# Performance work log

Measured on AMD Instinct MI355X. Metric: run time of the kernel, lower is better.

## Reference

```python
import jax, jax.numpy as jnp
import numpy as np

N_NODES = 1000000
N_EDGES = 2000000
N_FEAT = 11          # QM9 num_features
HIDDEN = 64
N_CLASSES = 19       # QM9 num_classes
BATCH = 128


def setup_inputs() -> dict:
    key = jax.random.key(0)
    k = jax.random.split(key, 8)
    x = jax.random.normal(k[0], (N_NODES, N_FEAT), dtype=jnp.float32)
    edge_index = jax.random.randint(k[1], (2, N_EDGES), 0, N_NODES, dtype=jnp.int64)
    y = jax.random.normal(k[2], (BATCH, N_CLASSES), dtype=jnp.float32)
    batch = jnp.sort(jax.random.randint(k[3], (N_NODES,), 0, BATCH, dtype=jnp.int64))
    # GCNConv params: weight [in, hidden], bias [hidden]
    W_conv = jax.random.normal(k[4], (N_FEAT, HIDDEN), dtype=jnp.float32) / np.sqrt(N_FEAT)
    b_conv = jnp.zeros((HIDDEN,), dtype=jnp.float32)
    # Final linear: [hidden, classes]
    W_lin = jax.random.normal(k[5], (HIDDEN, N_CLASSES), dtype=jnp.float32) / np.sqrt(HIDDEN)
    b_lin = jnp.zeros((N_CLASSES,), dtype=jnp.float32)
    return {"x": x, "edge_index": edge_index, "y": y, "batch": batch,
            "W_conv": W_conv, "b_conv": b_conv, "W_lin": W_lin, "b_lin": b_lin}


def reference(x, edge_index, y, batch, W_conv, b_conv, W_lin, b_lin):
    row, col = edge_index[0], edge_index[1]  # source -> target
    # GCN symmetric normalization (add_self_loops=False): deg over targets
    ones = jnp.ones((edge_index.shape[1],), dtype=x.dtype)
    deg = jax.ops.segment_sum(ones, col, num_segments=N_NODES)
    dinv = jnp.where(deg > 0, jax.lax.rsqrt(jnp.maximum(deg, 1.0)), 0.0)
    norm = dinv[row] * dinv[col]  # [E]
    # Transform then aggregate: gather at source, scatter-add at target
    xw = x @ W_conv                                    # [N, H]
    msgs = xw[row] * norm[:, None]                     # [E, H]
    agg = jax.ops.segment_sum(msgs, col, num_segments=N_NODES) + b_conv
    h = jax.nn.relu(agg)                               # [N, H]
    # global_mean_pool over batch ids (size=BATCH)
    summed = jax.ops.segment_sum(h, batch, num_segments=BATCH)   # [B, H]
    counts = jax.ops.segment_sum(jnp.ones((N_NODES,), dtype=x.dtype), batch, num_segments=BATCH)
    pooled = summed / jnp.maximum(counts, 1.0)[:, None]
    # dropout p=0.5 is identity in eval mode
    return pooled @ W_lin + b_lin                      # [B, classes]
```

## Files before the change

### kernel.cpp

```cpp
#include <hip/hip_runtime.h>

#define N_NODES   1000000
#define N_EDGES   2000000
#define N_FEAT    11
#define HIDDEN    64
#define BATCH     128
#define N_CLASSES 19

#define NPB     2048
#define NBUCK   489
#define BCAP    5120
#define EPB     8192
#define PBLK    245
#define NSLOT   8
#define NCHUNK  3907
#define FSTR    12

__device__ __forceinline__ unsigned f2b(float v) {
    unsigned u = __float_as_uint(v);
    return (u + 0x7FFFu + ((u >> 16) & 1u)) >> 16;
}

__global__ __launch_bounds__(1024) void part_kernel(const int* __restrict__ row,
                                                    const int* __restrict__ col,
                                                    int* __restrict__ bcnt,
                                                    int* __restrict__ part) {
    __shared__ int lh[512];
    const int t = threadIdx.x;
    if (t < 512) lh[t] = 0;
    __syncthreads();
    const int q0 = (blockIdx.x * EPB) >> 2;
    const int4* col4 = (const int4*)col;
    const int4* row4 = (const int4*)row;
    const int qa = q0 + t, qb = q0 + 1024 + t;
    const bool va = qa < N_EDGES / 4, vb = qb < N_EDGES / 4;
    int4 ca, ra, cb, rb;
    if (va) { ca = col4[qa]; ra = row4[qa]; }
    if (vb) { cb = col4[qb]; rb = row4[qb]; }
    if (va) {
        atomicAdd(&lh[ca.x >> 11], 1); atomicAdd(&lh[ca.y >> 11], 1);
        atomicAdd(&lh[ca.z >> 11], 1); atomicAdd(&lh[ca.w >> 11], 1);
    }
    if (vb) {
        atomicAdd(&lh[cb.x >> 11], 1); atomicAdd(&lh[cb.y >> 11], 1);
        atomicAdd(&lh[cb.z >> 11], 1); atomicAdd(&lh[cb.w >> 11], 1);
    }
    __syncthreads();
    if (t < NBUCK) {
        int v = lh[t];
        if (v) lh[t] = t * BCAP + atomicAdd(&bcnt[t], v);
    }
    __syncthreads();
    int p;
    if (va) {
        p = atomicAdd(&lh[ca.x >> 11], 1); part[p] = (ra.x << 11) | (ca.x & (NPB - 1));
        p = atomicAdd(&lh[ca.y >> 11], 1); part[p] = (ra.y << 11) | (ca.y & (NPB - 1));
        p = atomicAdd(&lh[ca.z >> 11], 1); part[p] = (ra.z << 11) | (ca.z & (NPB - 1));
        p = atomicAdd(&lh[ca.w >> 11], 1); part[p] = (ra.w << 11) | (ca.w & (NPB - 1));
    }
    if (vb) {
        p = atomicAdd(&lh[cb.x >> 11], 1); part[p] = (rb.x << 11) | (cb.x & (NPB - 1));
        p = atomicAdd(&lh[cb.y >> 11], 1); part[p] = (rb.y << 11) | (cb.y & (NPB - 1));
        p = atomicAdd(&lh[cb.z >> 11], 1); part[p] = (rb.z << 11) | (cb.z & (NPB - 1));
        p = atomicAdd(&lh[cb.w >> 11], 1); part[p] = (rb.w << 11) | (cb.w & (NPB - 1));
    }
}

__global__ __launch_bounds__(512) void sort2_kernel(const int* __restrict__ part,
                                                    const int* __restrict__ bcnt,
                                                    const float* __restrict__ x,
                                                    int* __restrict__ srcs,
                                                    int* __restrict__ nstart,
                                                    unsigned short* __restrict__ ndeg,
                                                    float* __restrict__ dinv,
                                                    unsigned short* __restrict__ xs) {
    __shared__ int cnt[NPB];
    __shared__ int off[NPB];
    __shared__ int tsum[512];
    __shared__ int stage[BCAP];
    const int t = threadIdx.x, b = blockIdx.x;
    for (int i = t; i < NPB; i += 512) cnt[i] = 0;
    __syncthreads();
    const int s0 = b * BCAP, e0 = s0 + bcnt[b];
    for (int j = s0 + t; j < e0; j += 512)
        atomicAdd(&cnt[part[j] & (NPB - 1)], 1);
    __syncthreads();
    const int i0 = t * 4;
    int c[4], s = 0;
#pragma unroll
    for (int q = 0; q < 4; ++q) { c[q] = cnt[i0 + q]; s += c[q]; }
    tsum[t] = s;
    __syncthreads();
    for (int o = 1; o < 512; o <<= 1) {
        int a = (t >= o) ? tsum[t - o] : 0;
        __syncthreads();
        tsum[t] += a;
        __syncthreads();
    }
    int run = tsum[t] - s;
#pragma unroll
    for (int q = 0; q < 4; ++q) { off[i0 + q] = run; run += c[q]; }
    __syncthreads();
    for (int i = t; i < NPB; i += 512) {
        int n = b * NPB + i;
        if (n < N_NODES) {
            int d = cnt[i];
            float dv = d ? rsqrtf((float)d) : 0.0f;
            dinv[n]   = dv;
            ndeg[n]   = (unsigned short)d;
            nstart[n] = s0 + off[i];
            const float* xr = x + (size_t)n * N_FEAT;
            unsigned h[11];
#pragma unroll
            for (int k = 0; k < 11; ++k) h[k] = f2b(dv * xr[k]);
            uint4 A, B;
            A.x = h[0] | (h[1] << 16); A.y = h[2] | (h[3] << 16);
            A.z = h[4] | (h[5] << 16); A.w = h[6] | (h[7] << 16);
            B.x = h[8] | (h[9] << 16); B.y = h[10]; B.z = 0u; B.w = 0u;
            uint4* o = (uint4*)(xs + (size_t)n * 16);
            o[0] = A; o[1] = B;
        }
    }
    __syncthreads();
    for (int j = s0 + t; j < e0; j += 512) {
        int p  = part[j];
        int cl = p & (NPB - 1);
        int pos = atomicAdd(&off[cl], 1);
        stage[pos] = p >> 11;
    }
    __syncthreads();
    const int m = e0 - s0;
    const int m4 = m >> 2;
    int4* d4 = (int4*)(srcs + s0);
    const int4* s4 = (const int4*)stage;
    for (int j = t; j < m4; j += 512) d4[j] = s4[j];
    for (int j = (m4 << 2) + t; j < m; j += 512) srcs[s0 + j] = stage[j];
}

__global__ __launch_bounds__(256) void gather_pool_kernel(
    const int* __restrict__ srcs, const unsigned short* __restrict__ xs,
    const int* __restrict__ nstart, const unsigned short* __restrict__ ndeg,
    const float* __restrict__ dinv, const int* __restrict__ batch,
    const float* __restrict__ Wc, const float* __restrict__ bc,
    float* __restrict__ pooled, float* __restrict__ countsf) {
    __shared__ float facc[256 * FSTR];
    __shared__ int   sj0[256];
    __shared__ int   sdeg[256];
    __shared__ float sdinv[256];
    __shared__ int   sbid[256];
    __shared__ int   sperm[256];
    __shared__ int   dcnt[32];
    __shared__ int   doff[32];
    __shared__ float pbuf[NSLOT * HIDDEN];
    __shared__ int   pcnt[NSLOT];
    const int t = threadIdx.x, lane = t & 63, w = t >> 6;
    const int base = blockIdx.x * 256;
    {
        int n = base + t;
        bool v = n < N_NODES;
        sj0[t]   = v ? nstart[n] : 0;
        sdeg[t]  = v ? (int)ndeg[n] : 0;
        sdinv[t] = v ? dinv[n] : 0.0f;
        sbid[t]  = v ? batch[n] : -1;
    }
    for (int i = t; i < NSLOT * HIDDEN; i += 256) pbuf[i] = 0.0f;
    if (t < NSLOT) pcnt[t] = 0;
    if (t < 32)    dcnt[t] = 0;
    __syncthreads();
    int mybin = sdeg[t] < 31 ? sdeg[t] : 31;
    atomicAdd(&dcnt[mybin], 1);
    __syncthreads();
    if (t < 32) {
        int r = 0;
        for (int i = 0; i < t; ++i) r += dcnt[i];
        doff[t] = r;
    }
    __syncthreads();
    int pos = atomicAdd(&doff[mybin], 1);
    sperm[pos] = t;
    __syncthreads();

    {
        int i  = sperm[t];
        int j0 = sj0[i], d = sdeg[i];
        float acc[11];
#pragma unroll
        for (int k = 0; k < 11; ++k) acc[k] = 0.0f;
        for (int j = j0; j < j0 + d; ++j) {
            int r = srcs[j];
            const uint4* xr = (const uint4*)(xs + (size_t)r * 16);
            uint4 A = xr[0];
            uint2 B = *(const uint2*)(xr + 1);
            acc[0]  += __uint_as_float(A.x << 16);
            acc[1]  += __uint_as_float(A.x & 0xFFFF0000u);
            acc[2]  += __uint_as_float(A.y << 16);
            acc[3]  += __uint_as_float(A.y & 0xFFFF0000u);
            acc[4]  += __uint_as_float(A.z << 16);
            acc[5]  += __uint_as_float(A.z & 0xFFFF0000u);
            acc[6]  += __uint_as_float(A.w << 16);
            acc[7]  += __uint_as_float(A.w & 0xFFFF0000u);
            acc[8]  += __uint_as_float(B.x << 16);
            acc[9]  += __uint_as_float(B.x & 0xFFFF0000u);
            acc[10] += __uint_as_float(B.y << 16);
        }
        float* f = &facc[i * FSTR];
#pragma unroll
        for (int k = 0; k < 11; ++k) f[k] = acc[k];
    }
    __syncthreads();

    float wk[N_FEAT];
#pragma unroll
    for (int k = 0; k < N_FEAT; ++k) wk[k] = Wc[k * HIDDEN + lane];
    const float bias = bc[lane];
    const int bid0 = sbid[0];
    int cur = -1; float accp = 0.0f; int cntp = 0;
    for (int i = w * 64; i < w * 64 + 64; ++i) {
        int bid = sbid[i];
        if (bid < 0) break;
        if (bid != cur) {
            if (cur >= 0) {
                int slot = cur - bid0;
                if (slot >= 0 && slot < NSLOT) {
                    atomicAdd(&pbuf[slot * HIDDEN + lane], accp);
                    if (lane == 0) atomicAdd(&pcnt[slot], cntp);
                } else {
                    atomicAdd(&pooled[(size_t)cur * HIDDEN + lane], accp);
                    if (lane == 0) atomicAdd(&countsf[cur], (float)cntp);
                }
            }
            cur = bid; accp = 0.0f; cntp = 0;
        }
        float s = 0.0f;
#pragma unroll
        for (int k = 0; k < N_FEAT; ++k)
            s = fmaf(wk[k], facc[i * FSTR + k], s);
        accp += fmaxf(fmaf(sdinv[i], s, bias), 0.0f);
        ++cntp;
    }
    if (cur >= 0) {
        int slot = cur - bid0;
        if (slot >= 0 && slot < NSLOT) {
            atomicAdd(&pbuf[slot * HIDDEN + lane], accp);
            if (lane == 0) atomicAdd(&pcnt[slot], cntp);
        } else {
            atomicAdd(&pooled[(size_t)cur * HIDDEN + lane], accp);
            if (lane == 0) atomicAdd(&countsf[cur], (float)cntp);
        }
    }
    __syncthreads();
    for (int s = w; s < NSLOT; s += 4) {
        int c = pcnt[s];
        if (c > 0) {
            atomicAdd(&pooled[(size_t)(bid0 + s) * HIDDEN + lane], pbuf[s * HIDDEN + lane]);
            if (lane == 0) atomicAdd(&countsf[bid0 + s], (float)c);
        }
    }
}

__global__ void final_kernel(const float* __restrict__ pooled, const float* __restrict__ counts,
                             const float* __restrict__ Wl, const float* __restrict__ bl,
                             float* __restrict__ out) {
    int i = blockIdx.x * blockDim.x + threadIdx.x;
    if (i >= BATCH * N_CLASSES) return;
    int b = i / N_CLASSES;
    int c = i - b * N_CLASSES;
    float inv = 1.0f / fmaxf(counts[b], 1.0f);
    float s = bl[c];
#pragma unroll 8
    for (int h = 0; h < HIDDEN; ++h)
        s = fmaf(pooled[b * HIDDEN + h] * inv, Wl[h * N_CLASSES + c], s);
    out[i] = s;
}

extern "C" void kernel_launch(void* const* d_in, const int* in_sizes, int n_in,
                              void* d_out, int out_size, void* d_ws, size_t ws_size,
                              hipStream_t stream) {
    const float* x     = (const float*)d_in[0];
    const int*   ei    = (const int*)d_in[1];
    const int*   batch = (const int*)d_in[3];
    const float* Wc    = (const float*)d_in[4];
    const float* bc    = (const float*)d_in[5];
    const float* Wl    = (const float*)d_in[6];
    const float* bl    = (const float*)d_in[7];
    float*       out   = (float*)d_out;

    int*            bcnt    = (int*)d_ws;
    float*          pooled  = (float*)(bcnt + 512);
    float*          countsf = pooled + BATCH * HIDDEN;
    unsigned short* xs      = (unsigned short*)(countsf + BATCH);
    int*            nstart  = (int*)(xs + (size_t)N_NODES * 16);
    unsigned short* ndeg    = (unsigned short*)(nstart + N_NODES);
    float*          dinv    = (float*)(ndeg + N_NODES);
    int*            part    = (int*)(dinv + N_NODES);
    int*            srcs    = part + (size_t)NBUCK * BCAP;

    size_t zero_bytes = (512 + BATCH * HIDDEN + BATCH) * 4;
    hipMemsetAsync(d_ws, 0, zero_bytes, stream);

    const int* row = ei;
    const int* col = ei + N_EDGES;

    part_kernel <<<PBLK, 1024, 0, stream>>>(row, col, bcnt, part);
    sort2_kernel<<<NBUCK, 512, 0, stream>>>(part, bcnt, x, srcs, nstart, ndeg, dinv, xs);
    gather_pool_kernel<<<NCHUNK, 256, 0, stream>>>(srcs, xs, nstart, ndeg, dinv,
                                                   batch, Wc, bc, pooled, countsf);
    final_kernel<<<(BATCH * N_CLASSES + 255) / 256, 256, 0, stream>>>(pooled, countsf, Wl, bl, out);
}
```

Before: 230.7 us.

## Compute per-node GCN transform with bf16 MFMA instead of scalar FMA loop

The per-block dense transform (aggregated 11 features times the 11x64 weight) now uses 16x16x32 bf16 MFMA tiles, with aggregated features packed to bf16 in shared memory and weights converted to bf16 per lane. Node counts are accumulated up front per node instead of per run. Pooling changes from per-wave run-length accumulation to per-element atomics into shared or global buffers, one atomic per node and channel. This adds bf16 rounding of the aggregates and weights, and many more atomics, in exchange for removing the scalar dot-product loop.

```diff
diff --git a/kernel.cpp b/kernel.cpp
--- a/kernel.cpp
+++ b/kernel.cpp
@@ -14,7 +14,11 @@
 #define PBLK    245
 #define NSLOT   8
 #define NCHUNK  3907
-#define FSTR    12
+#define FROW    24
+#define ZOFF    (256 * FROW)
+
+typedef __attribute__((ext_vector_type(8))) short v8s;
+typedef __attribute__((ext_vector_type(4))) float v4f;
 
 __device__ __forceinline__ unsigned f2b(float v) {
     unsigned u = __float_as_uint(v);
@@ -143,7 +147,7 @@
     const float* __restrict__ dinv, const int* __restrict__ batch,
     const float* __restrict__ Wc, const float* __restrict__ bc,
     float* __restrict__ pooled, float* __restrict__ countsf) {
-    __shared__ float facc[256 * FSTR];
+    __shared__ unsigned short fb16[ZOFF + 8];
     __shared__ int   sj0[256];
     __shared__ int   sdeg[256];
     __shared__ float sdinv[256];
@@ -154,6 +158,7 @@
     __shared__ float pbuf[NSLOT * HIDDEN];
     __shared__ int   pcnt[NSLOT];
     const int t = threadIdx.x, lane = t & 63, w = t >> 6;
+    const int quad = lane >> 4;
     const int base = blockIdx.x * 256;
     {
         int n = base + t;
@@ -166,7 +171,17 @@
     for (int i = t; i < NSLOT * HIDDEN; i += 256) pbuf[i] = 0.0f;
     if (t < NSLOT) pcnt[t] = 0;
     if (t < 32)    dcnt[t] = 0;
-    __syncthreads();
+    if (t < 4)     ((unsigned*)(fb16 + ZOFF))[t] = 0u;
+    __syncthreads();
+    const int bid0 = sbid[0];
+    {
+        int bid = sbid[t];
+        if (bid >= 0) {
+            int slot = bid - bid0;
+            if (slot >= 0 && slot < NSLOT) atomicAdd(&pcnt[slot], 1);
+            else atomicAdd(&countsf[bid], 1.0f);
+        }
+    }
     int mybin = sdeg[t] < 31 ? sdeg[t] : 31;
     atomicAdd(&dcnt[mybin], 1);
     __syncthreads();
@@ -203,49 +218,44 @@
             acc[9]  += __uint_as_float(B.x & 0xFFFF0000u);
             acc[10] += __uint_as_float(B.y << 16);
         }
-        float* f = &facc[i * FSTR];
-#pragma unroll
-        for (int k = 0; k < 11; ++k) f[k] = acc[k];
-    }
-    __syncthreads();
-
-    float wk[N_FEAT];
-#pragma unroll
-    for (int k = 0; k < N_FEAT; ++k) wk[k] = Wc[k * HIDDEN + lane];
-    const float bias = bc[lane];
-    const int bid0 = sbid[0];
-    int cur = -1; float accp = 0.0f; int cntp = 0;
-    for (int i = w * 64; i < w * 64 + 64; ++i) {
-        int bid = sbid[i];
-        if (bid < 0) break;
-        if (bid != cur) {
-            if (cur >= 0) {
-                int slot = cur - bid0;
-                if (slot >= 0 && slot < NSLOT) {
-                    atomicAdd(&pbuf[slot * HIDDEN + lane], accp);
-                    if (lane == 0) atomicAdd(&pcnt[slot], cntp);
-                } else {
-                    atomicAdd(&pooled[(size_t)cur * HIDDEN + lane], accp);
-                    if (lane == 0) atomicAdd(&countsf[cur], (float)cntp);
-                }
+        unsigned hb[11];
+#pragma unroll
+        for (int k = 0; k < 11; ++k) hb[k] = f2b(acc[k]);
+        uint4 U0, U1;
+        U0.x = hb[0] | (hb[1] << 16); U0.y = hb[2]  | (hb[3] << 16);
+        U0.z = hb[4] | (hb[5] << 16); U0.w = hb[6]  | (hb[7] << 16);
+        U1.x = hb[8] | (hb[9] << 16); U1.y = hb[10]; U1.z = 0u; U1.w = 0u;
+        uint4* wp = (uint4*)(fb16 + i * FROW);
+        wp[0] = U0; wp[1] = U1;
+    }
+    __syncthreads();
+
+    const int wbase = w * 16;
+    const int nch   = wbase + (lane & 15);
+    union { v8s v; unsigned short us[8]; } bf;
+#pragma unroll
+    for (int j = 0; j < 8; ++j) {
+        int k = quad * 8 + j;
+        bf.us[j] = (k < 11) ? (unsigned short)f2b(Wc[k * HIDDEN + nch]) : (unsigned short)0;
+    }
+    const float bias_lane = bc[nch];
+#pragma unroll 4
+    for (int mtile = 0; mtile < 16; ++mtile) {
+        const v8s* ap = (quad < 2)
+            ? (const v8s*)(fb16 + (mtile * 16 + (lane & 15)) * FROW + quad * 8)
+            : (const v8s*)(fb16 + ZOFF);
+        v8s a = *ap;
+        v4f d = __builtin_amdgcn_mfma_f32_16x16x32_bf16(a, bf.v, (v4f){0.f, 0.f, 0.f, 0.f}, 0, 0, 0);
+#pragma unroll
+        for (int r = 0; r < 4; ++r) {
+            int node = mtile * 16 + quad * 4 + r;
+            int bid  = sbid[node];
+            if (bid >= 0) {
+                float h = fmaxf(fmaf(sdinv[node], d[r], bias_lane), 0.0f);
+                int slot = bid - bid0;
+                if (slot >= 0 && slot < NSLOT) atomicAdd(&pbuf[slot * HIDDEN + nch], h);
+                else atomicAdd(&pooled[(size_t)bid * HIDDEN + nch], h);
             }
-            cur = bid; accp = 0.0f; cntp = 0;
-        }
-        float s = 0.0f;
-#pragma unroll
-        for (int k = 0; k < N_FEAT; ++k)
-            s = fmaf(wk[k], facc[i * FSTR + k], s);
-        accp += fmaxf(fmaf(sdinv[i], s, bias), 0.0f);
-        ++cntp;
-    }
-    if (cur >= 0) {
-        int slot = cur - bid0;
-        if (slot >= 0 && slot < NSLOT) {
-            atomicAdd(&pbuf[slot * HIDDEN + lane], accp);
-            if (lane == 0) atomicAdd(&pcnt[slot], cntp);
-        } else {
-            atomicAdd(&pooled[(size_t)cur * HIDDEN + lane], accp);
-            if (lane == 0) atomicAdd(&countsf[cur], (float)cntp);
         }
     }
     __syncthreads();
```

New measurement: 514.0 us. 2.23x slower.
